# Optimization experiments

Measured on AMD Instinct MI355X. Metric: run time of the kernel, lower is better.

## Reference

```python
import jax, jax.numpy as jnp
import numpy as np

R = 3                 # search_radius
S2 = (2 * R + 1) ** 2  # 49 correlation channels
VIS_PIXEL_SCALE = 0.1  # arcsec / pixel


def _interp_tokens(tokens, sh, sw, dh, dw):
    # tokens [B, N, D] on (sh, sw) grid -> (dh, dw) grid
    B, N, D = tokens.shape
    x = jnp.transpose(tokens, (0, 2, 1)).reshape(B, D, sh, sw)
    if (sh, sw) != (dh, dw):
        # torch F.interpolate bilinear align_corners=False == jax half-pixel bilinear
        x = jax.image.resize(x, (B, D, dh, dw), method='bilinear')
    return x  # [B, D, dh, dw]


def _l2norm(x, eps=1e-12):
    n = jnp.sqrt(jnp.sum(x * x, axis=1, keepdims=True))
    return x / jnp.maximum(n, eps)


def _corr_volume(q, ref):
    # q, ref: [B, D, H, W]; local cosine-similarity volume [B, S2, H, W]
    q = _l2norm(q)
    ref = _l2norm(ref)
    B, D, H, W = q.shape
    refp = jnp.pad(ref, ((0, 0), (0, 0), (R, R), (R, R)), mode='edge')  # replicate pad
    slices = [
        jnp.sum(q * jax.lax.dynamic_slice(refp, (0, 0, R + dy, R + dx), (B, D, H, W)), axis=1)
        for dy in range(-R, R + 1) for dx in range(-R, R + 1)
    ]
    return jnp.stack(slices, axis=1)


def _conv5(x, w, b):
    y = jax.lax.conv_general_dilated(x, w, (1, 1), 'SAME',
                                     dimension_numbers=('NCHW', 'OIHW', 'NCHW'))
    return y + b[None, :, None, None]


def _refine_net(x, w0, b0, w1, b1, w2, b2):
    h = jax.nn.gelu(_conv5(x, w0, b0), approximate=False)
    h = jax.nn.gelu(_conv5(h, w1, b1), approximate=False)
    return _conv5(h, w2, b2)


def setup_inputs() -> dict:
    key = jax.random.key(0)
    ks = jax.random.split(key, 8)
    B, D = 4, 256
    rubin_tokens = jax.random.normal(ks[0], (B, 64 * 64, D), dtype=jnp.float32)
    vis_tokens = jax.random.normal(ks[1], (B, 128 * 128, D), dtype=jnp.float32)
    in_ch = 2 + S2 + 1  # 52
    hid = 32
    def kaiming(k, shape):
        fan_in = shape[1] * shape[2] * shape[3]
        return jax.random.normal(k, shape, dtype=jnp.float32) / np.sqrt(fan_in)
    w0 = kaiming(ks[2], (hid, in_ch, 5, 5)); b0 = jnp.zeros((hid,), jnp.float32)
    w1 = kaiming(ks[3], (hid, hid, 5, 5));   b1 = jnp.zeros((hid,), jnp.float32)
    w2 = kaiming(ks[4], (2, hid, 5, 5));     b2 = jnp.zeros((2,), jnp.float32)
    log_temp = jnp.asarray(np.log(0.1), dtype=jnp.float32)
    return {
        'rubin_tokens': rubin_tokens, 'vis_tokens': vis_tokens,
        'w0': w0, 'b0': b0, 'w1': w1, 'b1': b1, 'w2': w2, 'b2': b2,
        'log_temp': log_temp,
        'rubin_h': 64, 'rubin_w': 64, 'vis_h': 128, 'vis_w': 128,
        'img_h': 2048, 'img_w': 2048,
    }


def reference(rubin_tokens, vis_tokens, w0, b0, w1, b1, w2, b2, log_temp,
              rubin_h, rubin_w, vis_h, vis_w, img_h, img_w):
    Hc, Wc = max(rubin_h, vis_h), max(rubin_w, vis_w)
    q = _interp_tokens(rubin_tokens, rubin_h, rubin_w, Hc, Wc)  # [B,D,Hc,Wc]
    k = _interp_tokens(vis_tokens, vis_h, vis_w, Hc, Wc)
    corr = _corr_volume(q, k)  # [B,S2,Hc,Wc]

    # soft-argmax over the (2R+1)^2 neighborhood
    coords = jnp.arange(-R, R + 1, dtype=corr.dtype)
    cy, cx = jnp.meshgrid(coords, coords, indexing='ij')
    cy = cy.reshape(1, S2, 1, 1)
    cx = cx.reshape(1, S2, 1, 1)
    temp = jnp.exp(log_temp)
    weights = jax.nn.softmax(corr / temp, axis=1)
    dy = jnp.sum(weights * cy, axis=1, keepdims=True)
    dx = jnp.sum(weights * cx, axis=1, keepdims=True)
    confidence = jnp.max(weights, axis=1, keepdims=True)
    raw_offsets = jnp.concatenate([dy, dx], axis=1)  # [B,2,Hc,Wc]

    x = jnp.concatenate([raw_offsets, corr, confidence], axis=1)  # [B,52,Hc,Wc]
    residual = _refine_net(x, w0, b0, w1, b1, w2, b2)
    refined = raw_offsets + residual

    sky_per_token_y = img_h * VIS_PIXEL_SCALE / Hc
    sky_per_token_x = img_w * VIS_PIXEL_SCALE / Wc
    dra = refined[:, 1:2] * sky_per_token_x
    ddec = refined[:, 0:1] * sky_per_token_y
    # [B,5,Hc,Wc]: dra, ddec, raw_dy, raw_dx, confidence
    return jnp.concatenate([dra, ddec, dy, dx, confidence], axis=1)
```

## Files before the change

### kernel.cpp

```cpp
#include <hip/hip_runtime.h>
#include <math.h>

#define Hh 128
#define Ww 128
#define Dd 256
#define Bb 4
#define HW (Hh*Ww)
#define NPIX (Bb*HW)
#define WP 132

typedef __attribute__((ext_vector_type(8))) short s16x8;
typedef __attribute__((ext_vector_type(4))) float f32x4;

__device__ __forceinline__ unsigned short f2bf(float f) {
    unsigned u = __float_as_uint(f);
    u += 0x7FFF + ((u >> 16) & 1);
    return (unsigned short)(u >> 16);
}

__device__ __forceinline__ float gelu_exact(float v) {
    return 0.5f * v * (1.0f + erff(v * 0.70710678118654752f));
}

__device__ __forceinline__ void ring_yx(int i, int& y, int& x) {
    if (i < 264) { y = i / 132; x = i - y * 132; }
    else if (i < 528) { int j = i - 264; int r = j / 132; y = 130 + r; x = j - r * 132; }
    else { int j = i - 528; y = 2 + (j >> 2); int m = j & 3; x = (m < 2) ? m : 128 + m; }
}

__global__ __launch_bounds__(256) void setup_norm(const float* __restrict__ w0,
                                                  const float* __restrict__ w1,
                                                  const float* __restrict__ w2,
                                                  unsigned short* __restrict__ wb0,
                                                  unsigned short* __restrict__ wb1,
                                                  unsigned short* __restrict__ wb2,
                                                  unsigned short* __restrict__ xbp,
                                                  unsigned short* __restrict__ h1p,
                                                  unsigned short* __restrict__ h2p,
                                                  const float* __restrict__ vis,
                                                  const float* __restrict__ rub,
                                                  unsigned short* __restrict__ kn,
                                                  unsigned short* __restrict__ qn) {
    __shared__ float stok[36 * 260];
    int tid = threadIdx.x;
    int blk = blockIdx.x;
    if (blk < 610) {
        int t = blk * 256 + tid;
        if (t < 66560) {
            uint4 z = (uint4){0, 0, 0, 0};
            if (t < 33280) {
                int img = t / 8320; int r = t - img * 8320; int px = r >> 3, g = r & 7;
                int y, x; ring_yx(px, y, x);
                *(uint4*)(xbp + ((size_t)(img * WP + y) * WP + x) * 64 + g * 8) = z;
            } else {
                int u = t - 33280;
                unsigned short* base = (u < 16640) ? h1p : h2p;
                int v = (u < 16640) ? u : u - 16640;
                int img = v / 4160; int r = v - img * 4160; int px = r >> 2, g = r & 3;
                int y, x; ring_yx(px, y, x);
                *(uint4*)(base + ((size_t)(img * WP + y) * WP + x) * 32 + g * 8) = z;
            }
            return;
        }
        int u = t - 66560;
        if (u < 51200) {
            int tap = u >> 11; int r = u & 2047; int n = r >> 6; int k = r & 63;
            wb0[u] = (k < 52) ? f2bf(w0[n * 1300 + k * 25 + tap]) : (unsigned short)0;
        } else if (u < 76800) {
            int v = u - 51200; int tap = v >> 10; int r = v & 1023; int n = r >> 5; int k = r & 31;
            wb1[v] = f2bf(w1[n * 800 + k * 25 + tap]);
        } else if (u < 89600) {
            int v = u - 76800; int tap = v >> 9; int r = v & 511; int n = r >> 5; int k = r & 31;
            wb2[v] = (n < 2) ? f2bf(w2[n * 800 + k * 25 + tap]) : (unsigned short)0;
        }
        return;
    }
    int nb = blk - 610;
    int g32 = tid >> 5, l = tid & 31;
    if (nb < 4096) {
        int pix0 = nb * 16 + g32 * 2;
        const float* base0 = vis + (size_t)pix0 * Dd + l * 4;
        float4 a0 = *(const float4*)(base0);
        float4 b0 = *(const float4*)(base0 + 128);
        float4 a1 = *(const float4*)(base0 + 256);
        float4 b1 = *(const float4*)(base0 + 384);
        float ss0 = a0.x * a0.x + a0.y * a0.y + a0.z * a0.z + a0.w * a0.w +
                    b0.x * b0.x + b0.y * b0.y + b0.z * b0.z + b0.w * b0.w;
        float ss1 = a1.x * a1.x + a1.y * a1.y + a1.z * a1.z + a1.w * a1.w +
                    b1.x * b1.x + b1.y * b1.y + b1.z * b1.z + b1.w * b1.w;
#pragma unroll
        for (int o = 1; o <= 16; o <<= 1) {
            ss0 += __shfl_xor(ss0, o, 64);
            ss1 += __shfl_xor(ss1, o, 64);
        }
        float inv0 = __builtin_amdgcn_rsqf(fmaxf(ss0, 1e-24f));
        float inv1 = __builtin_amdgcn_rsqf(fmaxf(ss1, 1e-24f));
        uint4 o0, o1;
        o0.x = f2bf(a0.x * inv0) | ((unsigned)f2bf(a0.y * inv0) << 16);
        o0.y = f2bf(a0.z * inv0) | ((unsigned)f2bf(a0.w * inv0) << 16);
        o0.z = f2bf(b0.x * inv0) | ((unsigned)f2bf(b0.y * inv0) << 16);
        o0.w = f2bf(b0.z * inv0) | ((unsigned)f2bf(b0.w * inv0) << 16);
        o1.x = f2bf(a1.x * inv1) | ((unsigned)f2bf(a1.y * inv1) << 16);
        o1.y = f2bf(a1.z * inv1) | ((unsigned)f2bf(a1.w * inv1) << 16);
        o1.z = f2bf(b1.x * inv1) | ((unsigned)f2bf(b1.y * inv1) << 16);
        o1.w = f2bf(b1.z * inv1) | ((unsigned)f2bf(b1.w * inv1) << 16);
        *(uint4*)(kn + (size_t)pix0 * Dd + l * 8) = o0;
        *(uint4*)(kn + (size_t)(pix0 + 1) * Dd + l * 8) = o1;
    } else {
        int blk2 = nb - 4096;
        int b = blk2 >> 8;
        int rem = blk2 & 255;
        int ty = rem >> 4, tx = rem & 15;
        int oy0 = ty * 8, ox0 = tx * 8;
        int rb = ty * 4 - 1, cb = tx * 4 - 1;
#pragma unroll
        for (int i = 0; i < 9; i++) {
            int g = i * 256 + tid;
            int t = g >> 6, c = g & 63;
            int jy = t / 6, jx = t - jy * 6;
            int gy = min(max(rb + jy, 0), 63);
            int gx = min(max(cb + jx, 0), 63);
            *(float4*)&stok[t * 260 + c * 4] =
                *(const float4*)(rub + ((size_t)(b * 4096 + gy * 64 + gx)) * 256 + c * 4);
        }
        __syncthreads();
        for (int k = 0; k < 8; k++) {
            int pp = g32 * 8 + k;
            int r = pp >> 3, c2 = pp & 7;
            int yo = oy0 + r, xo = ox0 + c2;
            float sy = 0.5f * yo - 0.25f, sx = 0.5f * xo - 0.25f;
            float fyf = floorf(sy), fxf = floorf(sx);
            float fy = sy - fyf, fx = sx - fxf;
            int jy0 = (int)fyf - rb, jx0 = (int)fxf - cb;
            const float* t00 = &stok[(jy0 * 6 + jx0) * 260];
            const float* t01 = t00 + 260;
            const float* t10 = t00 + 6 * 260;
            const float* t11 = t10 + 260;
            float w00 = (1.f - fy) * (1.f - fx), w01 = (1.f - fy) * fx;
            float w10 = fy * (1.f - fx), w11 = fy * fx;
            float4 av, bv;
            {
                float4 A0 = *(const float4*)(t00 + l * 4);
                float4 B0 = *(const float4*)(t01 + l * 4);
                float4 C0 = *(const float4*)(t10 + l * 4);
                float4 D0 = *(const float4*)(t11 + l * 4);
                av.x = w00 * A0.x + w01 * B0.x + w10 * C0.x + w11 * D0.x;
                av.y = w00 * A0.y + w01 * B0.y + w10 * C0.y + w11 * D0.y;
                av.z = w00 * A0.z + w01 * B0.z + w10 * C0.z + w11 * D0.z;
                av.w = w00 * A0.w + w01 * B0.w + w10 * C0.w + w11 * D0.w;
                float4 A1 = *(const float4*)(t00 + 128 + l * 4);
                float4 B1 = *(const float4*)(t01 + 128 + l * 4);
                float4 C1 = *(const float4*)(t10 + 128 + l * 4);
                float4 D1 = *(const float4*)(t11 + 128 + l * 4);
                bv.x = w00 * A1.x + w01 * B1.x + w10 * C1.x + w11 * D1.x;
                bv.y = w00 * A1.y + w01 * B1.y + w10 * C1.y + w11 * D1.y;
                bv.z = w00 * A1.z + w01 * B1.z + w10 * C1.z + w11 * D1.z;
                bv.w = w00 * A1.w + w01 * B1.w + w10 * C1.w + w11 * D1.w;
            }
            float ss = av.x * av.x + av.y * av.y + av.z * av.z + av.w * av.w +
                       bv.x * bv.x + bv.y * bv.y + bv.z * bv.z + bv.w * bv.w;
#pragma unroll
            for (int o = 1; o <= 16; o <<= 1) ss += __shfl_xor(ss, o, 64);
            float inv = __builtin_amdgcn_rsqf(fmaxf(ss, 1e-24f));
            size_t pix = (size_t)(b << 14) + yo * 128 + xo;
            uint4 o4;
            o4.x = f2bf(av.x * inv) | ((unsigned)f2bf(av.y * inv) << 16);
            o4.y = f2bf(av.z * inv) | ((unsigned)f2bf(av.w * inv) << 16);
            o4.z = f2bf(bv.x * inv) | ((unsigned)f2bf(bv.y * inv) << 16);
            o4.w = f2bf(bv.z * inv) | ((unsigned)f2bf(bv.w * inv) << 16);
            *(uint4*)(qn + pix * Dd + l * 8) = o4;
        }
    }
}

__global__ __launch_bounds__(512, 4) void corr_block(const unsigned short* __restrict__ qn,
                                                     const unsigned short* __restrict__ kn,
                                                     const float* __restrict__ log_temp,
                                                     unsigned short* __restrict__ xb,
                                                     float* __restrict__ out) {
    __shared__ __align__(16) char smem[320 * 144];
    unsigned* sC = (unsigned*)smem;
    int tid = threadIdx.x;
    int wid = tid >> 6, lane = tid & 63, l15 = lane & 15, quad = lane >> 4;
    int blk = blockIdx.x;
    int b = blk >> 7, rem = blk & 127;
    int y0 = (rem >> 3) << 3, x0 = (rem & 7) << 4;
    int y = y0 + wid;

    int soff[5], dstf[5];
#pragma unroll
    for (int i = 0; i < 5; i++) {
        int g = i * 512 + tid;
        int px = g >> 3, sub = g & 7;
        int pxc = min(px, 307);
        int ry = pxc / 22, rx = pxc - ry * 22;
        int yy = min(max(y0 - 3 + ry, 0), 127);
        int xx = min(max(x0 - 3 + rx, 0), 127);
        soff[i] = ((b << 14) + yy * 128 + xx) * 256 + sub * 8;
        dstf[i] = px * 144 + sub * 16;
    }
    int lpixoff[10];
#pragma unroll
    for (int f = 0; f < 10; f++) {
        int p = min(f * 16 + l15, 153);
        int pr = p / 22, pc = p - pr * 22;
        lpixoff[f] = ((wid + pr) * 22 + pc) * 144 + quad * 16;
    }
    int aoff = ((b << 14) + y * 128 + x0 + l15) * 256 + quad * 8;

    f32x4 acc[10];
#pragma unroll
    for (int f = 0; f < 10; f++) acc[f] = (f32x4){0.f, 0.f, 0.f, 0.f};

    uint4 st0 = *(const uint4*)(kn + soff[0]);
    uint4 st1 = *(const uint4*)(kn + soff[1]);
    uint4 st2 = *(const uint4*)(kn + soff[2]);
    uint4 st3 = *(const uint4*)(kn + soff[3]);
    uint4 st4 = *(const uint4*)(kn + soff[4]);
    s16x8 a0 = *(const s16x8*)(qn + aoff);
    s16x8 a1 = *(const s16x8*)(qn + aoff + 32);
    for (int c4 = 0; c4 < 4; c4++) {
        uint4 w0 = st0, w1 = st1, w2 = st2, w3 = st3, w4 = st4;
        s16x8 wa0 = a0, wa1 = a1;
        if (c4 < 3) {
            int co = (c4 + 1) * 64;
            st0 = *(const uint4*)(kn + soff[0] + co);
            st1 = *(const uint4*)(kn + soff[1] + co);
            st2 = *(const uint4*)(kn + soff[2] + co);
            st3 = *(const uint4*)(kn + soff[3] + co);
            st4 = *(const uint4*)(kn + soff[4] + co);
            a0 = *(const s16x8*)(qn + aoff + co);
            a1 = *(const s16x8*)(qn + aoff + co + 32);
        }
        __syncthreads();
        *(uint4*)(smem + dstf[0]) = w0;
        *(uint4*)(smem + dstf[1]) = w1;
        *(uint4*)(smem + dstf[2]) = w2;
        *(uint4*)(smem + dstf[3]) = w3;
        *(uint4*)(smem + dstf[4]) = w4;
        __syncthreads();
#pragma unroll
        for (int f = 0; f < 10; f++) {
            s16x8 bf = *(const s16x8*)(smem + lpixoff[f]);
            acc[f] = __builtin_amdgcn_mfma_f32_16x16x32_bf16(wa0, bf, acc[f], 0, 0, 0);
        }
#pragma unroll
        for (int f = 0; f < 10; f++) {
            s16x8 bf = *(const s16x8*)(smem + lpixoff[f] + 64);
            acc[f] = __builtin_amdgcn_mfma_f32_16x16x32_bf16(wa1, bf, acc[f], 0, 0, 0);
        }
    }
    __syncthreads();

#pragma unroll
    for (int i = 0; i < 3; i++) {
        int g = i * 512 + tid;
        int px = g / 12, ch = 52 + g - (g / 12) * 12;
        sC[px * 65 + ch] = 0u;
    }

    float inv_temp = expf(-log_temp[0]);
    float vmax[4] = {-1e30f, -1e30f, -1e30f, -1e30f};
#pragma unroll
    for (int f = 0; f < 10; f++) {
        int n = f * 16 + l15;
        if (n <= 153) {
            int dy = n / 22 - 3;
            int rx = n - (dy + 3) * 22;
#pragma unroll
            for (int i = 0; i < 4; i++) {
                int m = quad * 4 + i;
                int dx = rx - m - 3;
                if ((unsigned)(dx + 3) <= 6u) vmax[i] = fmaxf(vmax[i], acc[f][i]);
            }
        }
    }
#pragma unroll
    for (int o = 1; o <= 8; o <<= 1) {
#pragma unroll
        for (int i = 0; i < 4; i++) vmax[i] = fmaxf(vmax[i], __shfl_xor(vmax[i], o, 64));
    }
    float se[4] = {0, 0, 0, 0}, sey[4] = {0, 0, 0, 0}, sex[4] = {0, 0, 0, 0}, emax[4] = {0, 0, 0, 0};
#pragma unroll
    for (int f = 0; f < 10; f++) {
        int n = f * 16 + l15;
        if (n <= 153) {
            int dy = n / 22 - 3;
            int rx = n - (dy + 3) * 22;
#pragma unroll
            for (int i = 0; i < 4; i++) {
                int m = quad * 4 + i;
                int dx = rx - m - 3;
                if ((unsigned)(dx + 3) <= 6u) {
                    float v = acc[f][i];
                    float e = expf((v - vmax[i]) * inv_temp);
                    se[i] += e;
                    sey[i] += e * (float)dy;
                    sex[i] += e * (float)dx;
                    emax[i] = fmaxf(emax[i], e);
                    sC[(wid * 16 + m) * 65 + 2 + (dy + 3) * 7 + (dx + 3)] = (unsigned)f2bf(v);
                }
            }
        }
    }
#pragma unroll
    for (int o = 1; o <= 8; o <<= 1) {
#pragma unroll
        for (int i = 0; i < 4; i++) {
            se[i] += __shfl_xor(se[i], o, 64);
            sey[i] += __shfl_xor(sey[i], o, 64);
            sex[i] += __shfl_xor(sex[i], o, 64);
            emax[i] = fmaxf(emax[i], __shfl_xor(emax[i], o, 64));
        }
    }
    if (l15 == 0) {
#pragma unroll
        for (int i = 0; i < 4; i++) {
            int m = quad * 4 + i;
            float inv_se = 1.0f / se[i];
            float dyv = sey[i] * inv_se, dxv = sex[i] * inv_se, conf = emax[i] * inv_se;
            int px = wid * 16 + m;
            sC[px * 65 + 0] = (unsigned)f2bf(dyv);
            sC[px * 65 + 1] = (unsigned)f2bf(dxv);
            sC[px * 65 + 51] = (unsigned)f2bf(conf);
            float* op = out + (size_t)b * 5 * HW + y * 128 + x0 + m;
            op[2 * HW] = dyv; op[3 * HW] = dxv; op[4 * HW] = conf;
        }
    }
    __syncthreads();
#pragma unroll
    for (int i = 0; i < 2; i++) {
        int t2 = i * 512 + tid;
        int px = t2 >> 3, seg = t2 & 7;
        const unsigned* sp = sC + px * 65 + seg * 8;
        uint4 o;
        o.x = sp[0] | (sp[1] << 16);
        o.y = sp[2] | (sp[3] << 16);
        o.z = sp[4] | (sp[5] << 16);
        o.w = sp[6] | (sp[7] << 16);
        unsigned short* dst = xb + ((size_t)(b * WP + y0 + (px >> 4) + 2) * WP + x0 + (px & 15) + 2) * 64 + seg * 8;
        *(uint4*)dst = o;
    }
}

template <int KS, int OC, bool GELU>
__global__ __launch_bounds__(512, 4) void conv_tile(const unsigned short* __restrict__ in,
                                                    const unsigned short* __restrict__ wb,
                                                    const float* __restrict__ bias,
                                                    unsigned short* __restrict__ outp) {
    constexpr int ICP = KS * 32;
    constexpr int NF = OC / 16;
    constexpr int ABYTES = 240 * 64;
    constexpr int WROWS = 25 * OC;
    constexpr int WGRAN = WROWS * 4;
    __shared__ char smem[ABYTES + WROWS * 64];
    int tid = threadIdx.x;
    int wv = tid >> 6, lane = tid & 63, l15 = lane & 15, quad = lane >> 4;
    int blk = blockIdx.x;
    int b = blk >> 7, rem = blk & 127;
    int ty = rem >> 3, tx = rem & 7;
    int y0 = ty * 8, x0 = tx * 16;

    f32x4 acc[NF];
#pragma unroll
    for (int g = 0; g < NF; g++) acc[g] = (f32x4){0.f, 0.f, 0.f, 0.f};

    for (int ks = 0; ks < KS; ks++) {
        __syncthreads();
#pragma unroll
        for (int i = 0; i < 2; i++) {
            int g = i * 512 + tid;
            if (g < 960) {
                int px = g >> 2, sub = g & 3;
                int r = px / 20, c = px - r * 20;
                *(uint4*)(smem + px * 64 + (((sub ^ (px >> 1)) & 3) << 4)) =
                    *(const uint4*)(in + ((size_t)(b * WP + y0 + r) * WP + x0 + c) * ICP + ks * 32 + sub * 8);
            }
        }
#pragma unroll
        for (int i = 0; i < (WGRAN + 511) / 512; i++) {
            int g = i * 512 + tid;
            if (g < WGRAN) {
                int nl = g >> 2, sub = g & 3;
                *(uint4*)(smem + ABYTES + nl * 64 + (((sub ^ (nl >> 1)) & 3) << 4)) =
                    *(const uint4*)(wb + (size_t)nl * ICP + ks * 32 + sub * 8);
            }
        }
        __syncthreads();
#pragma unroll
        for (int ky = 0; ky < 5; ky++) {
#pragma unroll
            for (int kx = 0; kx < 5; kx++) {
                int px = (wv + ky) * 20 + l15 + kx;
                s16x8 a = *(const s16x8*)(smem + px * 64 + (((quad ^ (px >> 1)) & 3) << 4));
#pragma unroll
                for (int g = 0; g < NF; g++) {
                    int row = (ky * 5 + kx) * OC + g * 16 + l15;
                    s16x8 bf = *(const s16x8*)(smem + ABYTES + row * 64 + (((quad ^ (row >> 1)) & 3) << 4));
                    acc[g] = __builtin_amdgcn_mfma_f32_16x16x32_bf16(a, bf, acc[g], 0, 0, 0);
                }
            }
        }
    }
    size_t orow = ((size_t)(b * WP + y0 + wv + 2) * WP + x0 + 2) * OC;
#pragma unroll
    for (int g = 0; g < NF; g++) {
        float bv = bias[g * 16 + l15];
#pragma unroll
        for (int r = 0; r < 4; r++) {
            int m = quad * 4 + r;
            float v = acc[g][r] + bv;
            if (GELU) v = gelu_exact(v);
            outp[orow + (size_t)m * OC + g * 16 + l15] = f2bf(v);
        }
    }
}

__global__ __launch_bounds__(512, 4) void conv_final_tile(const unsigned short* __restrict__ in,
                                                          const unsigned short* __restrict__ wb,
                                                          const float* __restrict__ bias,
                                                          float* __restrict__ out) {
    constexpr int ICP = 32, OC = 16;
    constexpr int ABYTES = 240 * 64;
    constexpr int WROWS = 25 * OC;
    constexpr int WGRAN = WROWS * 4;
    __shared__ char smem[ABYTES + WROWS * 64];
    int tid = threadIdx.x;
    int wv = tid >> 6, lane = tid & 63, l15 = lane & 15, quad = lane >> 4;
    int blk = blockIdx.x;
    int b = blk >> 7, rem = blk & 127;
    int ty = rem >> 3, tx = rem & 7;
    int y0 = ty * 8, x0 = tx * 16;

#pragma unroll
    for (int i = 0; i < 2; i++) {
        int g = i * 512 + tid;
        if (g < 960) {
            int px = g >> 2, sub = g & 3;
            int r = px / 20, c = px - r * 20;
            *(uint4*)(smem + px * 64 + (((sub ^ (px >> 1)) & 3) << 4)) =
                *(const uint4*)(in + ((size_t)(b * WP + y0 + r) * WP + x0 + c) * ICP + sub * 8);
        }
    }
#pragma unroll
    for (int i = 0; i < 4; i++) {
        int g = i * 512 + tid;
        if (g < WGRAN) {
            int nl = g >> 2, sub = g & 3;
            *(uint4*)(smem + ABYTES + nl * 64 + (((sub ^ (nl >> 1)) & 3) << 4)) =
                *(const uint4*)(wb + (size_t)nl * ICP + sub * 8);
        }
    }
    __syncthreads();
    f32x4 acc = (f32x4){0.f, 0.f, 0.f, 0.f};
#pragma unroll
    for (int ky = 0; ky < 5; ky++) {
#pragma unroll
        for (int kx = 0; kx < 5; kx++) {
            int px = (wv + ky) * 20 + l15 + kx;
            s16x8 a = *(const s16x8*)(smem + px * 64 + (((quad ^ (px >> 1)) & 3) << 4));
            int row = (ky * 5 + kx) * OC + l15;
            s16x8 bf = *(const s16x8*)(smem + ABYTES + row * 64 + (((quad ^ (row >> 1)) & 3) << 4));
            acc = __builtin_amdgcn_mfma_f32_16x16x32_bf16(a, bf, acc, 0, 0, 0);
        }
    }
    if (l15 < 2) {
        float bv = bias[l15];
#pragma unroll
        for (int r = 0; r < 4; r++) {
            int m = quad * 4 + r;
            size_t p5 = (size_t)b * 5 * HW + (y0 + wv) * Ww + x0 + m;
            float a = acc[r] + bv;
            if (l15 == 0) {
                float dyv = out[p5 + 2 * HW];
                out[p5 + HW] = (dyv + a) * 1.6f;
            } else {
                float dxv = out[p5 + 3 * HW];
                out[p5] = (dxv + a) * 1.6f;
            }
        }
    }
}

extern "C" void kernel_launch(void* const* d_in, const int* in_sizes, int n_in,
                              void* d_out, int out_size, void* d_ws, size_t ws_size,
                              hipStream_t stream) {
    const float* rub = (const float*)d_in[0];
    const float* vis = (const float*)d_in[1];
    const float* w0 = (const float*)d_in[2];
    const float* b0 = (const float*)d_in[3];
    const float* w1 = (const float*)d_in[4];
    const float* b1 = (const float*)d_in[5];
    const float* w2 = (const float*)d_in[6];
    const float* b2 = (const float*)d_in[7];
    const float* log_temp = (const float*)d_in[8];
    float* out = (float*)d_out;

    char* ws = (char*)d_ws;
    size_t off = 0;
    const size_t PADPIX = (size_t)Bb * WP * WP;
    unsigned short* kn = (unsigned short*)(ws + off); off += (size_t)NPIX * Dd * 2;
    unsigned short* qn = (unsigned short*)(ws + off); off += (size_t)NPIX * Dd * 2;
    unsigned short* xbp = (unsigned short*)(ws + off); off += PADPIX * 64 * 2;
    unsigned short* h1p = (unsigned short*)(ws + off); off += PADPIX * 32 * 2;
    unsigned short* h2p = (unsigned short*)(ws + off); off += PADPIX * 32 * 2;
    unsigned short* wb0 = (unsigned short*)(ws + off); off += 51200 * 2;
    unsigned short* wb1 = (unsigned short*)(ws + off); off += 25600 * 2;
    unsigned short* wb2 = (unsigned short*)(ws + off); off += 12800 * 2;

    setup_norm<<<5730, 256, 0, stream>>>(w0, w1, w2, wb0, wb1, wb2,
                                         xbp, h1p, h2p, vis, rub, kn, qn);
    corr_block<<<512, 512, 0, stream>>>(qn, kn, log_temp, xbp, out);
    conv_tile<2, 32, true><<<512, 512, 0, stream>>>(xbp, wb0, b0, h1p);
    conv_tile<1, 32, true><<<512, 512, 0, stream>>>(h1p, wb1, b1, h2p);
    conv_final_tile<<<512, 512, 0, stream>>>(h2p, wb2, b2, out);
}
```

Measured before the change: 195.0 us.

## Fuse query interpolation into correlation and merge last two convs

The bilinear upsampling and L2-normalisation of the rubin query tokens move into the correlation kernel. Each block stages the 64x64 token neighbourhood in shared memory and builds bf16 MFMA fragments in registers, scaling by the inverse norm after accumulation. This removes the full-resolution qn write and read. The second and third convolutions are also fused into one kernel that keeps the GELU hidden activations for a 20x12 halo tile in LDS, which needs a 4-pixel padded h1 buffer. In exchange, conv2 work is recomputed on the halo, LDS pressure rises, and the weights are reloaded in stages.

```diff
diff --git a/kernel.cpp b/kernel.cpp
--- a/kernel.cpp
+++ b/kernel.cpp
@@ -8,6 +8,7 @@
 #define HW (Hh*Ww)
 #define NPIX (Bb*HW)
 #define WP 132
+#define WP1 136
 
 typedef __attribute__((ext_vector_type(8))) short s16x8;
 typedef __attribute__((ext_vector_type(4))) float f32x4;
@@ -26,6 +27,12 @@
     if (i < 264) { y = i / 132; x = i - y * 132; }
     else if (i < 528) { int j = i - 264; int r = j / 132; y = 130 + r; x = j - r * 132; }
     else { int j = i - 528; y = 2 + (j >> 2); int m = j & 3; x = (m < 2) ? m : 128 + m; }
+}
+
+__device__ __forceinline__ void ring4_yx(int i, int& y, int& x) {
+    if (i < 544) { y = i / 136; x = i - y * 136; }
+    else if (i < 1088) { int j = i - 544; int r = j / 136; y = 132 + r; x = j - r * 136; }
+    else { int j = i - 1088; y = 4 + (j >> 3); int m = j & 7; x = (m < 4) ? m : 128 + m; }
 }
 
 __global__ __launch_bounds__(256) void setup_norm(const float* __restrict__ w0,
@@ -36,149 +43,78 @@
                                                   unsigned short* __restrict__ wb2,
                                                   unsigned short* __restrict__ xbp,
                                                   unsigned short* __restrict__ h1p,
-                                                  unsigned short* __restrict__ h2p,
                                                   const float* __restrict__ vis,
-                                                  const float* __restrict__ rub,
-                                                  unsigned short* __restrict__ kn,
-                                                  unsigned short* __restrict__ qn) {
-    __shared__ float stok[36 * 260];
+                                                  unsigned short* __restrict__ kn) {
     int tid = threadIdx.x;
     int blk = blockIdx.x;
-    if (blk < 610) {
+    if (blk < 612) {
         int t = blk * 256 + tid;
-        if (t < 66560) {
-            uint4 z = (uint4){0, 0, 0, 0};
-            if (t < 33280) {
-                int img = t / 8320; int r = t - img * 8320; int px = r >> 3, g = r & 7;
-                int y, x; ring_yx(px, y, x);
-                *(uint4*)(xbp + ((size_t)(img * WP + y) * WP + x) * 64 + g * 8) = z;
-            } else {
-                int u = t - 33280;
-                unsigned short* base = (u < 16640) ? h1p : h2p;
-                int v = (u < 16640) ? u : u - 16640;
-                int img = v / 4160; int r = v - img * 4160; int px = r >> 2, g = r & 3;
-                int y, x; ring_yx(px, y, x);
-                *(uint4*)(base + ((size_t)(img * WP + y) * WP + x) * 32 + g * 8) = z;
-            }
+        uint4 z = (uint4){0, 0, 0, 0};
+        if (t < 33280) {
+            int img = t / 8320; int r = t - img * 8320; int px = r >> 3, g = r & 7;
+            int y, x; ring_yx(px, y, x);
+            *(uint4*)(xbp + ((size_t)(img * WP + y) * WP + x) * 64 + g * 8) = z;
             return;
         }
-        int u = t - 66560;
+        if (t < 67072) {
+            int u2 = t - 33280;
+            int img = u2 / 8448; int r = u2 - img * 8448; int px = r >> 2, g = r & 3;
+            int y, x; ring4_yx(px, y, x);
+            *(uint4*)(h1p + ((size_t)(img * WP1 + y) * WP1 + x) * 32 + g * 8) = z;
+            return;
+        }
+        int u = t - 67072;
         if (u < 51200) {
             int tap = u >> 11; int r = u & 2047; int n = r >> 6; int k = r & 63;
             wb0[u] = (k < 52) ? f2bf(w0[n * 1300 + k * 25 + tap]) : (unsigned short)0;
         } else if (u < 76800) {
             int v = u - 51200; int tap = v >> 10; int r = v & 1023; int n = r >> 5; int k = r & 31;
             wb1[v] = f2bf(w1[n * 800 + k * 25 + tap]);
-        } else if (u < 89600) {
+        } else {
             int v = u - 76800; int tap = v >> 9; int r = v & 511; int n = r >> 5; int k = r & 31;
             wb2[v] = (n < 2) ? f2bf(w2[n * 800 + k * 25 + tap]) : (unsigned short)0;
         }
         return;
     }
-    int nb = blk - 610;
+    int nb = blk - 612;
     int g32 = tid >> 5, l = tid & 31;
-    if (nb < 4096) {
-        int pix0 = nb * 16 + g32 * 2;
-        const float* base0 = vis + (size_t)pix0 * Dd + l * 4;
-        float4 a0 = *(const float4*)(base0);
-        float4 b0 = *(const float4*)(base0 + 128);
-        float4 a1 = *(const float4*)(base0 + 256);
-        float4 b1 = *(const float4*)(base0 + 384);
-        float ss0 = a0.x * a0.x + a0.y * a0.y + a0.z * a0.z + a0.w * a0.w +
-                    b0.x * b0.x + b0.y * b0.y + b0.z * b0.z + b0.w * b0.w;
-        float ss1 = a1.x * a1.x + a1.y * a1.y + a1.z * a1.z + a1.w * a1.w +
-                    b1.x * b1.x + b1.y * b1.y + b1.z * b1.z + b1.w * b1.w;
-#pragma unroll
-        for (int o = 1; o <= 16; o <<= 1) {
-            ss0 += __shfl_xor(ss0, o, 64);
-            ss1 += __shfl_xor(ss1, o, 64);
-        }
-        float inv0 = __builtin_amdgcn_rsqf(fmaxf(ss0, 1e-24f));
-        float inv1 = __builtin_amdgcn_rsqf(fmaxf(ss1, 1e-24f));
-        uint4 o0, o1;
-        o0.x = f2bf(a0.x * inv0) | ((unsigned)f2bf(a0.y * inv0) << 16);
-        o0.y = f2bf(a0.z * inv0) | ((unsigned)f2bf(a0.w * inv0) << 16);
-        o0.z = f2bf(b0.x * inv0) | ((unsigned)f2bf(b0.y * inv0) << 16);
-        o0.w = f2bf(b0.z * inv0) | ((unsigned)f2bf(b0.w * inv0) << 16);
-        o1.x = f2bf(a1.x * inv1) | ((unsigned)f2bf(a1.y * inv1) << 16);
-        o1.y = f2bf(a1.z * inv1) | ((unsigned)f2bf(a1.w * inv1) << 16);
-        o1.z = f2bf(b1.x * inv1) | ((unsigned)f2bf(b1.y * inv1) << 16);
-        o1.w = f2bf(b1.z * inv1) | ((unsigned)f2bf(b1.w * inv1) << 16);
-        *(uint4*)(kn + (size_t)pix0 * Dd + l * 8) = o0;
-        *(uint4*)(kn + (size_t)(pix0 + 1) * Dd + l * 8) = o1;
-    } else {
-        int blk2 = nb - 4096;
-        int b = blk2 >> 8;
-        int rem = blk2 & 255;
-        int ty = rem >> 4, tx = rem & 15;
-        int oy0 = ty * 8, ox0 = tx * 8;
-        int rb = ty * 4 - 1, cb = tx * 4 - 1;
-#pragma unroll
-        for (int i = 0; i < 9; i++) {
-            int g = i * 256 + tid;
-            int t = g >> 6, c = g & 63;
-            int jy = t / 6, jx = t - jy * 6;
-            int gy = min(max(rb + jy, 0), 63);
-            int gx = min(max(cb + jx, 0), 63);
-            *(float4*)&stok[t * 260 + c * 4] =
-                *(const float4*)(rub + ((size_t)(b * 4096 + gy * 64 + gx)) * 256 + c * 4);
-        }
-        __syncthreads();
-        for (int k = 0; k < 8; k++) {
-            int pp = g32 * 8 + k;
-            int r = pp >> 3, c2 = pp & 7;
-            int yo = oy0 + r, xo = ox0 + c2;
-            float sy = 0.5f * yo - 0.25f, sx = 0.5f * xo - 0.25f;
-            float fyf = floorf(sy), fxf = floorf(sx);
-            float fy = sy - fyf, fx = sx - fxf;
-            int jy0 = (int)fyf - rb, jx0 = (int)fxf - cb;
-            const float* t00 = &stok[(jy0 * 6 + jx0) * 260];
-            const float* t01 = t00 + 260;
-            const float* t10 = t00 + 6 * 260;
-            const float* t11 = t10 + 260;
-            float w00 = (1.f - fy) * (1.f - fx), w01 = (1.f - fy) * fx;
-            float w10 = fy * (1.f - fx), w11 = fy * fx;
-            float4 av, bv;
-            {
-                float4 A0 = *(const float4*)(t00 + l * 4);
-                float4 B0 = *(const float4*)(t01 + l * 4);
-                float4 C0 = *(const float4*)(t10 + l * 4);
-                float4 D0 = *(const float4*)(t11 + l * 4);
-                av.x = w00 * A0.x + w01 * B0.x + w10 * C0.x + w11 * D0.x;
-                av.y = w00 * A0.y + w01 * B0.y + w10 * C0.y + w11 * D0.y;
-                av.z = w00 * A0.z + w01 * B0.z + w10 * C0.z + w11 * D0.z;
-                av.w = w00 * A0.w + w01 * B0.w + w10 * C0.w + w11 * D0.w;
-                float4 A1 = *(const float4*)(t00 + 128 + l * 4);
-                float4 B1 = *(const float4*)(t01 + 128 + l * 4);
-                float4 C1 = *(const float4*)(t10 + 128 + l * 4);
-                float4 D1 = *(const float4*)(t11 + 128 + l * 4);
-                bv.x = w00 * A1.x + w01 * B1.x + w10 * C1.x + w11 * D1.x;
-                bv.y = w00 * A1.y + w01 * B1.y + w10 * C1.y + w11 * D1.y;
-                bv.z = w00 * A1.z + w01 * B1.z + w10 * C1.z + w11 * D1.z;
-                bv.w = w00 * A1.w + w01 * B1.w + w10 * C1.w + w11 * D1.w;
-            }
-            float ss = av.x * av.x + av.y * av.y + av.z * av.z + av.w * av.w +
-                       bv.x * bv.x + bv.y * bv.y + bv.z * bv.z + bv.w * bv.w;
-#pragma unroll
-            for (int o = 1; o <= 16; o <<= 1) ss += __shfl_xor(ss, o, 64);
-            float inv = __builtin_amdgcn_rsqf(fmaxf(ss, 1e-24f));
-            size_t pix = (size_t)(b << 14) + yo * 128 + xo;
-            uint4 o4;
-            o4.x = f2bf(av.x * inv) | ((unsigned)f2bf(av.y * inv) << 16);
-            o4.y = f2bf(av.z * inv) | ((unsigned)f2bf(av.w * inv) << 16);
-            o4.z = f2bf(bv.x * inv) | ((unsigned)f2bf(bv.y * inv) << 16);
-            o4.w = f2bf(bv.z * inv) | ((unsigned)f2bf(bv.w * inv) << 16);
-            *(uint4*)(qn + pix * Dd + l * 8) = o4;
-        }
-    }
-}
-
-__global__ __launch_bounds__(512, 4) void corr_block(const unsigned short* __restrict__ qn,
+    int pix0 = nb * 16 + g32 * 2;
+    const float* base0 = vis + (size_t)pix0 * Dd + l * 4;
+    float4 a0 = *(const float4*)(base0);
+    float4 b0 = *(const float4*)(base0 + 128);
+    float4 a1 = *(const float4*)(base0 + 256);
+    float4 b1 = *(const float4*)(base0 + 384);
+    float ss0 = a0.x * a0.x + a0.y * a0.y + a0.z * a0.z + a0.w * a0.w +
+                b0.x * b0.x + b0.y * b0.y + b0.z * b0.z + b0.w * b0.w;
+    float ss1 = a1.x * a1.x + a1.y * a1.y + a1.z * a1.z + a1.w * a1.w +
+                b1.x * b1.x + b1.y * b1.y + b1.z * b1.z + b1.w * b1.w;
+#pragma unroll
+    for (int o = 1; o <= 16; o <<= 1) {
+        ss0 += __shfl_xor(ss0, o, 64);
+        ss1 += __shfl_xor(ss1, o, 64);
+    }
+    float inv0 = __builtin_amdgcn_rsqf(fmaxf(ss0, 1e-24f));
+    float inv1 = __builtin_amdgcn_rsqf(fmaxf(ss1, 1e-24f));
+    uint4 o0, o1;
+    o0.x = f2bf(a0.x * inv0) | ((unsigned)f2bf(a0.y * inv0) << 16);
+    o0.y = f2bf(a0.z * inv0) | ((unsigned)f2bf(a0.w * inv0) << 16);
+    o0.z = f2bf(b0.x * inv0) | ((unsigned)f2bf(b0.y * inv0) << 16);
+    o0.w = f2bf(b0.z * inv0) | ((unsigned)f2bf(b0.w * inv0) << 16);
+    o1.x = f2bf(a1.x * inv1) | ((unsigned)f2bf(a1.y * inv1) << 16);
+    o1.y = f2bf(a1.z * inv1) | ((unsigned)f2bf(a1.w * inv1) << 16);
+    o1.z = f2bf(b1.x * inv1) | ((unsigned)f2bf(b1.y * inv1) << 16);
+    o1.w = f2bf(b1.z * inv1) | ((unsigned)f2bf(b1.w * inv1) << 16);
+    *(uint4*)(kn + (size_t)pix0 * Dd + l * 8) = o0;
+    *(uint4*)(kn + (size_t)(pix0 + 1) * Dd + l * 8) = o1;
+}
+
+__global__ __launch_bounds__(512, 4) void corr_block(const float* __restrict__ rub,
                                                      const unsigned short* __restrict__ kn,
                                                      const float* __restrict__ log_temp,
                                                      unsigned short* __restrict__ xb,
                                                      float* __restrict__ out) {
-    __shared__ __align__(16) char smem[320 * 144];
+    __shared__ __align__(16) char smem[62400];
+    float* stok = (float*)smem;
     unsigned* sC = (unsigned*)smem;
     int tid = threadIdx.x;
     int wid = tid >> 6, lane = tid & 63, l15 = lane & 15, quad = lane >> 4;
@@ -186,6 +122,20 @@
     int b = blk >> 7, rem = blk & 127;
     int y0 = (rem >> 3) << 3, x0 = (rem & 7) << 4;
     int y = y0 + wid;
+    int ry0 = (y0 >> 1) - 1, cx0 = (x0 >> 1) - 1;
+
+#pragma unroll
+    for (int i = 0; i < 8; i++) {
+        int g = i * 512 + tid;
+        if (g < 3840) {
+            int t = g >> 6, c = g & 63;
+            int jy = t / 10, jxx = t - jy * 10;
+            int gy = min(max(ry0 + jy, 0), 63);
+            int gx = min(max(cx0 + jxx, 0), 63);
+            *(float4*)&stok[t * 260 + c * 4] =
+                *(const float4*)(rub + ((size_t)(b * 4096 + gy * 64 + gx)) * 256 + c * 4);
+        }
+    }
 
     int soff[5], dstf[5];
 #pragma unroll
@@ -206,22 +156,62 @@
         int pr = p / 22, pc = p - pr * 22;
         lpixoff[f] = ((wid + pr) * 22 + pc) * 144 + quad * 16;
     }
-    int aoff = ((b << 14) + y * 128 + x0 + l15) * 256 + quad * 8;
-
-    f32x4 acc[10];
-#pragma unroll
-    for (int f = 0; f < 10; f++) acc[f] = (f32x4){0.f, 0.f, 0.f, 0.f};
-
     uint4 st0 = *(const uint4*)(kn + soff[0]);
     uint4 st1 = *(const uint4*)(kn + soff[1]);
     uint4 st2 = *(const uint4*)(kn + soff[2]);
     uint4 st3 = *(const uint4*)(kn + soff[3]);
     uint4 st4 = *(const uint4*)(kn + soff[4]);
-    s16x8 a0 = *(const s16x8*)(qn + aoff);
-    s16x8 a1 = *(const s16x8*)(qn + aoff + 32);
+
+    __syncthreads();
+
+    s16x8 afr[8];
+    float inv;
+    {
+        int xq = x0 + l15;
+        float sy = 0.5f * y - 0.25f, sx = 0.5f * xq - 0.25f;
+        float fyf = floorf(sy), fxf = floorf(sx);
+        float fy = sy - fyf, fx = sx - fxf;
+        int iy = (int)fyf - ry0, jx = (int)fxf - cx0;
+        const float* tb = &stok[(iy * 10 + jx) * 260];
+        float w00 = (1.f - fy) * (1.f - fx), w01 = (1.f - fy) * fx;
+        float w10 = fy * (1.f - fx), w11 = fy * fx;
+        float ss = 0.f;
+#pragma unroll
+        for (int j = 0; j < 8; j++) {
+            int f0 = j * 16 + quad * 4;
+            float4 A0 = *(const float4*)(tb + f0);
+            float4 A1 = *(const float4*)(tb + 128 + f0);
+            float4 B0 = *(const float4*)(tb + 260 + f0);
+            float4 B1 = *(const float4*)(tb + 388 + f0);
+            float4 C0 = *(const float4*)(tb + 2600 + f0);
+            float4 C1 = *(const float4*)(tb + 2728 + f0);
+            float4 D0 = *(const float4*)(tb + 2860 + f0);
+            float4 D1 = *(const float4*)(tb + 2988 + f0);
+            float v0 = w00 * A0.x + w01 * B0.x + w10 * C0.x + w11 * D0.x;
+            float v1 = w00 * A0.y + w01 * B0.y + w10 * C0.y + w11 * D0.y;
+            float v2 = w00 * A0.z + w01 * B0.z + w10 * C0.z + w11 * D0.z;
+            float v3 = w00 * A0.w + w01 * B0.w + w10 * C0.w + w11 * D0.w;
+            float v4 = w00 * A1.x + w01 * B1.x + w10 * C1.x + w11 * D1.x;
+            float v5 = w00 * A1.y + w01 * B1.y + w10 * C1.y + w11 * D1.y;
+            float v6 = w00 * A1.z + w01 * B1.z + w10 * C1.z + w11 * D1.z;
+            float v7 = w00 * A1.w + w01 * B1.w + w10 * C1.w + w11 * D1.w;
+            ss += v0 * v0 + v1 * v1 + v2 * v2 + v3 * v3 +
+                  v4 * v4 + v5 * v5 + v6 * v6 + v7 * v7;
+            unsigned short* fp = (unsigned short*)&afr[j];
+            fp[0] = f2bf(v0); fp[1] = f2bf(v1); fp[2] = f2bf(v2); fp[3] = f2bf(v3);
+            fp[4] = f2bf(v4); fp[5] = f2bf(v5); fp[6] = f2bf(v6); fp[7] = f2bf(v7);
+        }
+        ss += __shfl_xor(ss, 16, 64);
+        ss += __shfl_xor(ss, 32, 64);
+        inv = __builtin_amdgcn_rsqf(fmaxf(ss, 1e-24f));
+    }
+
+    f32x4 acc[10];
+#pragma unroll
+    for (int f = 0; f < 10; f++) acc[f] = (f32x4){0.f, 0.f, 0.f, 0.f};
+
     for (int c4 = 0; c4 < 4; c4++) {
         uint4 w0 = st0, w1 = st1, w2 = st2, w3 = st3, w4 = st4;
-        s16x8 wa0 = a0, wa1 = a1;
         if (c4 < 3) {
             int co = (c4 + 1) * 64;
             st0 = *(const uint4*)(kn + soff[0] + co);
@@ -229,8 +219,6 @@
             st2 = *(const uint4*)(kn + soff[2] + co);
             st3 = *(const uint4*)(kn + soff[3] + co);
             st4 = *(const uint4*)(kn + soff[4] + co);
-            a0 = *(const s16x8*)(qn + aoff + co);
-            a1 = *(const s16x8*)(qn + aoff + co + 32);
         }
         __syncthreads();
         *(uint4*)(smem + dstf[0]) = w0;
@@ -239,6 +227,7 @@
         *(uint4*)(smem + dstf[3]) = w3;
         *(uint4*)(smem + dstf[4]) = w4;
         __syncthreads();
+        s16x8 wa0 = afr[2 * c4], wa1 = afr[2 * c4 + 1];
 #pragma unroll
         for (int f = 0; f < 10; f++) {
             s16x8 bf = *(const s16x8*)(smem + lpixoff[f]);
@@ -250,6 +239,16 @@
             acc[f] = __builtin_amdgcn_mfma_f32_16x16x32_bf16(wa1, bf, acc[f], 0, 0, 0);
         }
     }
+
+    float invm[4];
+#pragma unroll
+    for (int i = 0; i < 4; i++) invm[i] = __shfl(inv, quad * 4 + i, 16);
+#pragma unroll
+    for (int f = 0; f < 10; f++) {
+#pragma unroll
+        for (int i = 0; i < 4; i++) acc[f][i] *= invm[i];
+    }
+
     __syncthreads();
 
 #pragma unroll
@@ -343,12 +342,11 @@
     }
 }
 
-template <int KS, int OC, bool GELU>
-__global__ __launch_bounds__(512, 4) void conv_tile(const unsigned short* __restrict__ in,
-                                                    const unsigned short* __restrict__ wb,
-                                                    const float* __restrict__ bias,
-                                                    unsigned short* __restrict__ outp) {
-    constexpr int ICP = KS * 32;
+__global__ __launch_bounds__(512, 4) void conv1_tile(const unsigned short* __restrict__ in,
+                                                     const unsigned short* __restrict__ wb,
+                                                     const float* __restrict__ bias,
+                                                     unsigned short* __restrict__ outp) {
+    constexpr int KS = 2, OC = 32, ICP = 64;
     constexpr int NF = OC / 16;
     constexpr int ABYTES = 240 * 64;
     constexpr int WROWS = 25 * OC;
@@ -402,29 +400,29 @@
             }
         }
     }
-    size_t orow = ((size_t)(b * WP + y0 + wv + 2) * WP + x0 + 2) * OC;
+    size_t orow = ((size_t)(b * WP1 + y0 + wv + 4) * WP1 + x0 + 4) * OC;
 #pragma unroll
     for (int g = 0; g < NF; g++) {
         float bv = bias[g * 16 + l15];
 #pragma unroll
         for (int r = 0; r < 4; r++) {
             int m = quad * 4 + r;
-            float v = acc[g][r] + bv;
-            if (GELU) v = gelu_exact(v);
+            float v = gelu_exact(acc[g][r] + bv);
             outp[orow + (size_t)m * OC + g * 16 + l15] = f2bf(v);
         }
     }
 }
 
-__global__ __launch_bounds__(512, 4) void conv_final_tile(const unsigned short* __restrict__ in,
-                                                          const unsigned short* __restrict__ wb,
-                                                          const float* __restrict__ bias,
-                                                          float* __restrict__ out) {
-    constexpr int ICP = 32, OC = 16;
-    constexpr int ABYTES = 240 * 64;
-    constexpr int WROWS = 25 * OC;
-    constexpr int WGRAN = WROWS * 4;
-    __shared__ char smem[ABYTES + WROWS * 64];
+__global__ __launch_bounds__(512, 4) void conv2_final(const unsigned short* __restrict__ h1,
+                                                      const unsigned short* __restrict__ wb1,
+                                                      const float* __restrict__ b1,
+                                                      const unsigned short* __restrict__ wb2,
+                                                      const float* __restrict__ b2,
+                                                      float* __restrict__ out) {
+    constexpr int H1B = 384 * 64;
+    constexpr int WOFF = H1B;
+    constexpr int H2OFF = H1B + 26624;
+    __shared__ __align__(16) char smem[66560];
     int tid = threadIdx.x;
     int wv = tid >> 6, lane = tid & 63, l15 = lane & 15, quad = lane >> 4;
     int blk = blockIdx.x;
@@ -432,45 +430,129 @@
     int ty = rem >> 3, tx = rem & 7;
     int y0 = ty * 8, x0 = tx * 16;
 
-#pragma unroll
-    for (int i = 0; i < 2; i++) {
-        int g = i * 512 + tid;
-        if (g < 960) {
-            int px = g >> 2, sub = g & 3;
-            int r = px / 20, c = px - r * 20;
-            *(uint4*)(smem + px * 64 + (((sub ^ (px >> 1)) & 3) << 4)) =
-                *(const uint4*)(in + ((size_t)(b * WP + y0 + r) * WP + x0 + c) * ICP + sub * 8);
-        }
+    int p0u = wv * 16 + l15;
+    int p1u = (8 + wv) * 16 + l15;
+    int r0 = p0u / 20, c0 = p0u - r0 * 20;
+    int r1 = p1u / 20, c1 = p1u - r1 * 20;
+    bool has1 = ((8 + wv) < 15);
+
+#pragma unroll
+    for (int i = 0; i < 3; i++) {
+        int g = i * 512 + tid;
+        int px = g >> 2, sub = g & 3;
+        int r = px / 24, c = px - r * 24;
+        *(uint4*)(smem + px * 64 + (((sub ^ (px >> 1)) & 3) << 4)) =
+            *(const uint4*)(h1 + ((size_t)(b * WP1 + y0 + r) * WP1 + x0 + c) * 32 + sub * 8);
     }
 #pragma unroll
     for (int i = 0; i < 4; i++) {
         int g = i * 512 + tid;
-        if (g < WGRAN) {
+        if (g < 1664) {
             int nl = g >> 2, sub = g & 3;
-            *(uint4*)(smem + ABYTES + nl * 64 + (((sub ^ (nl >> 1)) & 3) << 4)) =
-                *(const uint4*)(wb + (size_t)nl * ICP + sub * 8);
-        }
-    }
-    __syncthreads();
-    f32x4 acc = (f32x4){0.f, 0.f, 0.f, 0.f};
-#pragma unroll
-    for (int ky = 0; ky < 5; ky++) {
-#pragma unroll
-        for (int kx = 0; kx < 5; kx++) {
-            int px = (wv + ky) * 20 + l15 + kx;
+            *(uint4*)(smem + WOFF + nl * 64 + (((sub ^ (nl >> 1)) & 3) << 4)) =
+                *(const uint4*)(wb1 + (size_t)nl * 32 + sub * 8);
+        }
+    }
+    __syncthreads();
+
+    f32x4 acc2[2][2];
+#pragma unroll
+    for (int s = 0; s < 2; s++) { acc2[s][0] = (f32x4){0,0,0,0}; acc2[s][1] = (f32x4){0,0,0,0}; }
+
+    for (int t = 0; t < 13; t++) {
+        int tap = t, ky = tap / 5, kx = tap - ky * 5;
+        int lr0 = t * 32 + l15, lr1 = t * 32 + 16 + l15;
+        s16x8 wf0 = *(const s16x8*)(smem + WOFF + lr0 * 64 + (((quad ^ (lr0 >> 1)) & 3) << 4));
+        s16x8 wf1 = *(const s16x8*)(smem + WOFF + lr1 * 64 + (((quad ^ (lr1 >> 1)) & 3) << 4));
+        {
+            int px = (r0 + ky) * 24 + c0 + kx;
             s16x8 a = *(const s16x8*)(smem + px * 64 + (((quad ^ (px >> 1)) & 3) << 4));
-            int row = (ky * 5 + kx) * OC + l15;
-            s16x8 bf = *(const s16x8*)(smem + ABYTES + row * 64 + (((quad ^ (row >> 1)) & 3) << 4));
-            acc = __builtin_amdgcn_mfma_f32_16x16x32_bf16(a, bf, acc, 0, 0, 0);
-        }
+            acc2[0][0] = __builtin_amdgcn_mfma_f32_16x16x32_bf16(a, wf0, acc2[0][0], 0, 0, 0);
+            acc2[0][1] = __builtin_amdgcn_mfma_f32_16x16x32_bf16(a, wf1, acc2[0][1], 0, 0, 0);
+        }
+        if (has1) {
+            int px = (r1 + ky) * 24 + c1 + kx;
+            s16x8 a = *(const s16x8*)(smem + px * 64 + (((quad ^ (px >> 1)) & 3) << 4));
+            acc2[1][0] = __builtin_amdgcn_mfma_f32_16x16x32_bf16(a, wf0, acc2[1][0], 0, 0, 0);
+            acc2[1][1] = __builtin_amdgcn_mfma_f32_16x16x32_bf16(a, wf1, acc2[1][1], 0, 0, 0);
+        }
+    }
+    __syncthreads();
+#pragma unroll
+    for (int i = 0; i < 3; i++) {
+        int g = i * 512 + tid;
+        int nl = g >> 2, sub = g & 3;
+        *(uint4*)(smem + WOFF + nl * 64 + (((sub ^ (nl >> 1)) & 3) << 4)) =
+            *(const uint4*)(wb1 + (size_t)(416 + nl) * 32 + sub * 8);
+    }
+    __syncthreads();
+    for (int t = 0; t < 12; t++) {
+        int tap = 13 + t, ky = tap / 5, kx = tap - ky * 5;
+        int lr0 = t * 32 + l15, lr1 = t * 32 + 16 + l15;
+        s16x8 wf0 = *(const s16x8*)(smem + WOFF + lr0 * 64 + (((quad ^ (lr0 >> 1)) & 3) << 4));
+        s16x8 wf1 = *(const s16x8*)(smem + WOFF + lr1 * 64 + (((quad ^ (lr1 >> 1)) & 3) << 4));
+        {
+            int px = (r0 + ky) * 24 + c0 + kx;
+            s16x8 a = *(const s16x8*)(smem + px * 64 + (((quad ^ (px >> 1)) & 3) << 4));
+            acc2[0][0] = __builtin_amdgcn_mfma_f32_16x16x32_bf16(a, wf0, acc2[0][0], 0, 0, 0);
+            acc2[0][1] = __builtin_amdgcn_mfma_f32_16x16x32_bf16(a, wf1, acc2[0][1], 0, 0, 0);
+        }
+        if (has1) {
+            int px = (r1 + ky) * 24 + c1 + kx;
+            s16x8 a = *(const s16x8*)(smem + px * 64 + (((quad ^ (px >> 1)) & 3) << 4));
+            acc2[1][0] = __builtin_amdgcn_mfma_f32_16x16x32_bf16(a, wf0, acc2[1][0], 0, 0, 0);
+            acc2[1][1] = __builtin_amdgcn_mfma_f32_16x16x32_bf16(a, wf1, acc2[1][1], 0, 0, 0);
+        }
+    }
+#pragma unroll
+    for (int s = 0; s < 2; s++) {
+        int u = s * 8 + wv;
+        if (u < 15) {
+#pragma unroll
+            for (int g2 = 0; g2 < 2; g2++) {
+                float bvv = b1[g2 * 16 + l15];
+                int n = g2 * 16 + l15, gran = n >> 3;
+#pragma unroll
+                for (int rr = 0; rr < 4; rr++) {
+                    int p = u * 16 + quad * 4 + rr;
+                    int r2 = p / 20, c2 = p - r2 * 20;
+                    int gy = y0 - 2 + r2, gx = x0 - 2 + c2;
+                    float v = gelu_exact(acc2[s][g2][rr] + bvv);
+                    unsigned short o = ((unsigned)gy < 128u && (unsigned)gx < 128u)
+                                           ? f2bf(v) : (unsigned short)0;
+                    *(unsigned short*)(smem + H2OFF + p * 64 +
+                                       (((gran ^ (p >> 1)) & 3) << 4) + (n & 7) * 2) = o;
+                }
+            }
+        }
+    }
+    __syncthreads();
+#pragma unroll
+    for (int i = 0; i < 4; i++) {
+        int g = i * 512 + tid;
+        if (g < 1600) {
+            int nl = g >> 2, sub = g & 3;
+            *(uint4*)(smem + WOFF + nl * 64 + (((sub ^ (nl >> 1)) & 3) << 4)) =
+                *(const uint4*)(wb2 + (size_t)nl * 32 + sub * 8);
+        }
+    }
+    __syncthreads();
+    f32x4 acc3 = (f32x4){0.f, 0.f, 0.f, 0.f};
+    for (int t = 0; t < 25; t++) {
+        int ky = t / 5, kx = t - ky * 5;
+        int p3 = (wv + ky) * 20 + l15 + kx;
+        s16x8 a = *(const s16x8*)(smem + H2OFF + p3 * 64 + (((quad ^ (p3 >> 1)) & 3) << 4));
+        int lr = t * 16 + l15;
+        s16x8 bf = *(const s16x8*)(smem + WOFF + lr * 64 + (((quad ^ (lr >> 1)) & 3) << 4));
+        acc3 = __builtin_amdgcn_mfma_f32_16x16x32_bf16(a, bf, acc3, 0, 0, 0);
     }
     if (l15 < 2) {
-        float bv = bias[l15];
-#pragma unroll
-        for (int r = 0; r < 4; r++) {
-            int m = quad * 4 + r;
+        float bv = b2[l15];
+#pragma unroll
+        for (int rr = 0; rr < 4; rr++) {
+            int m = quad * 4 + rr;
             size_t p5 = (size_t)b * 5 * HW + (y0 + wv) * Ww + x0 + m;
-            float a = acc[r] + bv;
+            float a = acc3[rr] + bv;
             if (l15 == 0) {
                 float dyv = out[p5 + 2 * HW];
                 out[p5 + HW] = (dyv + a) * 1.6f;
@@ -499,19 +581,17 @@
     char* ws = (char*)d_ws;
     size_t off = 0;
     const size_t PADPIX = (size_t)Bb * WP * WP;
+    const size_t PADPIX1 = (size_t)Bb * WP1 * WP1;
     unsigned short* kn = (unsigned short*)(ws + off); off += (size_t)NPIX * Dd * 2;
-    unsigned short* qn = (unsigned short*)(ws + off); off += (size_t)NPIX * Dd * 2;
     unsigned short* xbp = (unsigned short*)(ws + off); off += PADPIX * 64 * 2;
-    unsigned short* h1p = (unsigned short*)(ws + off); off += PADPIX * 32 * 2;
-    unsigned short* h2p = (unsigned short*)(ws + off); off += PADPIX * 32 * 2;
+    unsigned short* h1p = (unsigned short*)(ws + off); off += PADPIX1 * 32 * 2;
     unsigned short* wb0 = (unsigned short*)(ws + off); off += 51200 * 2;
     unsigned short* wb1 = (unsigned short*)(ws + off); off += 25600 * 2;
     unsigned short* wb2 = (unsigned short*)(ws + off); off += 12800 * 2;
 
-    setup_norm<<<5730, 256, 0, stream>>>(w0, w1, w2, wb0, wb1, wb2,
-                                         xbp, h1p, h2p, vis, rub, kn, qn);
-    corr_block<<<512, 512, 0, stream>>>(qn, kn, log_temp, xbp, out);
-    conv_tile<2, 32, true><<<512, 512, 0, stream>>>(xbp, wb0, b0, h1p);
-    conv_tile<1, 32, true><<<512, 512, 0, stream>>>(h1p, wb1, b1, h2p);
-    conv_final_tile<<<512, 512, 0, stream>>>(h2p, wb2, b2, out);
-}
+    setup_norm<<<4708, 256, 0, stream>>>(w0, w1, w2, wb0, wb1, wb2,
+                                         xbp, h1p, vis, kn);
+    corr_block<<<512, 512, 0, stream>>>(rub, kn, log_temp, xbp, out);
+    conv1_tile<<<512, 512, 0, stream>>>(xbp, wb0, b0, h1p);
+    conv2_final<<<512, 512, 0, stream>>>(h1p, wb1, b1, wb2, b2, out);
+}
```

After: 228.9 us. 17.4% more time.
